# Kernel tuning notes

Measured on AMD Instinct MI355X. Metric: run time of the kernel, lower is better.

## Reference

```python
import jax, jax.numpy as jnp
import numpy as np

EMBED = 768
HEADS = 12
HEAD_DIM = EMBED // HEADS
FFN = 4 * EMBED
EPS = 1e-5


def setup_inputs() -> dict:
    key = jax.random.key(0)
    ks = jax.random.split(key, 12)
    s = 0.02
    inp = {
        'x': jax.random.normal(ks[0], (1, 4096, EMBED), dtype=jnp.float32),
        'Wq': jax.random.normal(ks[1], (EMBED, EMBED), dtype=jnp.float32) * s,
        'bq': jnp.zeros((EMBED,), jnp.float32),
        'Wk': jax.random.normal(ks[2], (EMBED, EMBED), dtype=jnp.float32) * s,
        'bk': jnp.zeros((EMBED,), jnp.float32),
        'Wv': jax.random.normal(ks[3], (EMBED, EMBED), dtype=jnp.float32) * s,
        'bv': jnp.zeros((EMBED,), jnp.float32),
        'Wo': jax.random.normal(ks[4], (EMBED, EMBED), dtype=jnp.float32) * s,
        'bo': jnp.zeros((EMBED,), jnp.float32),
        'ln1_g': jnp.ones((EMBED,), jnp.float32),
        'ln1_b': jnp.zeros((EMBED,), jnp.float32),
        'W1': jax.random.normal(ks[5], (EMBED, FFN), dtype=jnp.float32) * s,
        'b1': jnp.zeros((FFN,), jnp.float32),
        'W2': jax.random.normal(ks[6], (FFN, EMBED), dtype=jnp.float32) * s,
        'b2': jnp.zeros((EMBED,), jnp.float32),
        'ln2_g': jnp.ones((EMBED,), jnp.float32),
        'ln2_b': jnp.zeros((EMBED,), jnp.float32),
    }
    return inp


def _layernorm(x, g, b):
    mu = jnp.mean(x, axis=-1, keepdims=True)
    var = jnp.mean(jnp.square(x - mu), axis=-1, keepdims=True)
    return (x - mu) * jax.lax.rsqrt(var + EPS) * g + b


def reference(x, Wq, bq, Wk, bk, Wv, bv, Wo, bo, ln1_g, ln1_b, W1, b1, W2, b2, ln2_g, ln2_b):
    B, S, D = x.shape
    # QKV projections -> [B, H, S, d]
    def split_heads(t):
        return t.reshape(B, S, HEADS, HEAD_DIM).transpose(0, 2, 1, 3)
    q = split_heads(x @ Wq + bq)
    k = split_heads(x @ Wk + bk)
    v = split_heads(x @ Wv + bv)
    scores = jnp.einsum('bhqd,bhkd->bhqk', q, k) / np.sqrt(HEAD_DIM).astype(np.float32)
    attn = jax.nn.softmax(scores, axis=-1)
    ctx = jnp.einsum('bhqk,bhkd->bhqd', attn, v)
    ctx = ctx.transpose(0, 2, 1, 3).reshape(B, S, D)
    attn_out = ctx @ Wo + bo
    h = _layernorm(x + attn_out, ln1_g, ln1_b)
    ffn = jax.nn.gelu(h @ W1 + b1, approximate=False) @ W2 + b2
    return _layernorm(h + ffn, ln2_g, ln2_b)
```

## Files before the change

kernel.cpp:

```cpp
#include <hip/hip_runtime.h>
#include <hip/hip_bf16.h>

typedef __attribute__((ext_vector_type(8))) short s16x8;
typedef __attribute__((ext_vector_type(4))) int   i32x4;
typedef __attribute__((ext_vector_type(4))) float f32x4;
typedef __attribute__((ext_vector_type(8))) __bf16 bf16x8;

__device__ __forceinline__ short f2bf(float f) {
  unsigned u = __builtin_bit_cast(unsigned, f);
  u = (u + 0x7FFFu + ((u >> 16) & 1u)) >> 16;
  return (short)u;
}
__device__ __forceinline__ float bf2f(short s) {
  unsigned u = ((unsigned)(unsigned short)s) << 16;
  return __builtin_bit_cast(float, u);
}
__device__ __forceinline__ f32x4 mfma16(s16x8 a, s16x8 b, f32x4 c) {
  return __builtin_amdgcn_mfma_f32_16x16x32_bf16(
      __builtin_bit_cast(bf16x8, a), __builtin_bit_cast(bf16x8, b), c, 0, 0, 0);
}
__device__ __forceinline__ void gload16(const void* g, void* l) {
  __builtin_amdgcn_global_load_lds(
      (const __attribute__((address_space(1))) void*)g,
      (__attribute__((address_space(3))) void*)l, 16, 0, 0);
}

__global__ __launch_bounds__(256) void convert_x_kernel(const float* __restrict__ src,
                                                        short* __restrict__ dst, int n8) {
  int i = blockIdx.x * 256 + threadIdx.x;
  if (i >= n8) return;
  float4 v0 = ((const float4*)src)[i * 2];
  float4 v1 = ((const float4*)src)[i * 2 + 1];
  s16x8 o;
  o[0] = f2bf(v0.x); o[1] = f2bf(v0.y); o[2] = f2bf(v0.z); o[3] = f2bf(v0.w);
  o[4] = f2bf(v1.x); o[5] = f2bf(v1.y); o[6] = f2bf(v1.z); o[7] = f2bf(v1.w);
  *(s16x8*)&dst[i * 8] = o;
}

__global__ __launch_bounds__(256) void bconcat_kernel(const float* __restrict__ bq,
                                                      const float* __restrict__ bk,
                                                      const float* __restrict__ bv,
                                                      float* __restrict__ out) {
  int i = blockIdx.x * 256 + threadIdx.x;
  if (i < 2304) out[i] = i < 768 ? bq[i] : (i < 1536 ? bk[i - 768] : bv[i - 1536]);
}

__global__ __launch_bounds__(256) void wconv_kernel(const float* __restrict__ src,
                                                    short* __restrict__ dst, int K, int N) {
  __shared__ float t[32][33];
  int n0 = blockIdx.x * 32, k0 = blockIdx.y * 32;
  int tx = threadIdx.x & 31, ty = threadIdx.x >> 5;
#pragma unroll
  for (int r = 0; r < 4; ++r) t[ty + r * 8][tx] = src[(long)(k0 + ty + r * 8) * N + n0 + tx];
  __syncthreads();
#pragma unroll
  for (int r = 0; r < 4; ++r)
    dst[(long)(n0 + ty + r * 8) * K + k0 + tx] = f2bf(t[tx][ty + r * 8]);
}

__global__ __launch_bounds__(256) void vtrans_kernel(const short* __restrict__ qkv,
                                                     short* __restrict__ vt) {
  __shared__ short t[32][34];
  int c0 = blockIdx.x * 32, s0 = blockIdx.y * 32;
  int tx = threadIdx.x & 31, ty = threadIdx.x >> 5;
#pragma unroll
  for (int r = 0; r < 4; ++r)
    t[ty + r * 8][tx] = qkv[(long)(s0 + ty + r * 8) * 2304 + 1536 + c0 + tx];
  __syncthreads();
#pragma unroll
  for (int r = 0; r < 4; ++r)
    vt[(long)(c0 + ty + r * 8) * 4096 + s0 + tx] = t[tx][ty + r * 8];
}

template <int OUT_MODE>
__global__ __launch_bounds__(256) void gemm_kernel(const short* __restrict__ A,
                                                   const short* __restrict__ Bt,
                                                   const float* __restrict__ bias,
                                                   void* __restrict__ Cout,
                                                   int M, int N, int Kfull, int Ksub) {
  __shared__ short As[128 * 32];
  __shared__ short Bs[128 * 32];
  const int tid = threadIdx.x;
  const int wave = tid >> 6, lane = tid & 63;
  const int lr = lane & 15, lg = lane >> 4;
  const int wm = wave >> 1, wn = wave & 1;
  const int bm = blockIdx.x, bn = blockIdx.y;
  const long koff = (long)blockIdx.z * Ksub;

  f32x4 acc[4][4] = {};

  const int r0 = tid >> 2;
  const int cc = (tid & 3) * 8;
  const short* Ag0 = A + (long)(bm * 128 + r0) * Kfull + koff + cc;
  const short* Ag1 = Ag0 + (long)64 * Kfull;
  const short* Bg0 = Bt + (long)(bn * 128 + r0) * Kfull + koff + cc;
  const short* Bg1 = Bg0 + (long)64 * Kfull;
  short* Asl0 = As + tid * 8;
  short* Asl1 = As + 64 * 32 + tid * 8;
  short* Bsl0 = Bs + tid * 8;
  short* Bsl1 = Bs + 64 * 32 + tid * 8;

  for (int k0 = 0; k0 < Ksub; k0 += 32) {
    __syncthreads();
    gload16(Ag0 + k0, Asl0);
    gload16(Ag1 + k0, Asl1);
    gload16(Bg0 + k0, Bsl0);
    gload16(Bg1 + k0, Bsl1);
    __syncthreads();
    s16x8 af[4], bfr[4];
#pragma unroll
    for (int m = 0; m < 4; ++m) {
      int row = wm * 64 + m * 16 + lr;
      af[m] = *(const s16x8*)&As[row * 32 + lg * 8];
    }
#pragma unroll
    for (int n = 0; n < 4; ++n) {
      int row = wn * 64 + n * 16 + lr;
      bfr[n] = *(const s16x8*)&Bs[row * 32 + lg * 8];
    }
#pragma unroll
    for (int m = 0; m < 4; ++m)
#pragma unroll
      for (int n = 0; n < 4; ++n)
        acc[m][n] = mfma16(af[m], bfr[n], acc[m][n]);
  }

  const int gr0 = bm * 128 + wm * 64 + lg * 4;
  const int gc0 = bn * 128 + wn * 64 + lr;
  float* outF = (float*)Cout + (long)blockIdx.z * M * N;
#pragma unroll
  for (int n = 0; n < 4; ++n) {
    int col = gc0 + n * 16;
    float bb = (blockIdx.z == 0) ? bias[col] : 0.f;
#pragma unroll
    for (int m = 0; m < 4; ++m) {
#pragma unroll
      for (int j = 0; j < 4; ++j) {
        int row = gr0 + m * 16 + j;
        float v = acc[m][n][j] + bb;
        if (OUT_MODE == 2) v = 0.5f * v * (1.0f + erff(v * 0.70710678118f));
        if (OUT_MODE == 1) outF[(long)row * N + col] = v;
        else ((short*)Cout)[(long)row * N + col] = f2bf(v);
      }
    }
  }
}

__global__ __launch_bounds__(256) void flash_kernel(const short* __restrict__ qkv,
                                                    const short* __restrict__ vt,
                                                    float* __restrict__ Opart,
                                                    float* __restrict__ Lpart) {
  __shared__ short Kt[64 * 72];
  __shared__ short Vs[64 * 72];
  __shared__ short Ps[128 * 72];
  const int tid = threadIdx.x;
  const int wave = tid >> 6, lane = tid & 63;
  const int lr = lane & 15, lg = lane >> 4;
  const int h = blockIdx.y, qb = blockIdx.x, sp = blockIdx.z;
  const int qc = h * 64;
  const int hc = 768 + h * 64;
  const int vr = h * 64;
  const float QSCALE = 0.125f * 1.44269504088896f;

#pragma unroll
  for (int i = 0; i < 4; ++i) {
    int c = tid + i * 256;
    int row = c >> 3, cq = (c & 7) * 8;
    *(i32x4*)&Ps[row * 72 + cq] =
        *(const i32x4*)&qkv[(long)(qb * 128 + row) * 2304 + qc + cq];
  }
  __syncthreads();
  s16x8 qf[2][2];
#pragma unroll
  for (int m = 0; m < 2; ++m)
#pragma unroll
    for (int ks = 0; ks < 2; ++ks) {
      int row = wave * 32 + m * 16 + lr;
      s16x8 v = *(const s16x8*)&Ps[row * 72 + ks * 32 + lg * 8];
#pragma unroll
      for (int e = 0; e < 8; ++e) {
        __bf16 b = (__bf16)(bf2f(v[e]) * QSCALE);
        v[e] = (short)__builtin_bit_cast(unsigned short, b);
      }
      qf[m][ks] = v;
    }

  float l_part[8];
#pragma unroll
  for (int i = 0; i < 8; ++i) l_part[i] = 0.f;
  f32x4 oacc[2][4] = {};

  for (int it = 0; it < 32; ++it) {
    const int s0 = sp * 2048 + it * 64;
    __syncthreads();
#pragma unroll
    for (int i = 0; i < 2; ++i) {
      int c = tid + i * 256;
      int row = c >> 3, cq = (c & 7) * 8;
      *(i32x4*)&Kt[row * 72 + cq] =
          *(const i32x4*)&qkv[(long)(s0 + row) * 2304 + hc + cq];
      *(i32x4*)&Vs[row * 72 + cq] =
          *(const i32x4*)&vt[(long)(vr + row) * 4096 + s0 + cq];
    }
    __syncthreads();
    f32x4 sacc[2][4] = {};
#pragma unroll
    for (int ks = 0; ks < 2; ++ks) {
      s16x8 kf[4];
#pragma unroll
      for (int n = 0; n < 4; ++n) {
        int row = n * 16 + lr;
        kf[n] = *(const s16x8*)&Kt[row * 72 + ks * 32 + lg * 8];
      }
      __builtin_amdgcn_s_setprio(1);
#pragma unroll
      for (int m = 0; m < 2; ++m)
#pragma unroll
        for (int n = 0; n < 4; ++n)
          sacc[m][n] = mfma16(qf[m][ks], kf[n], sacc[m][n]);
      __builtin_amdgcn_s_setprio(0);
    }
#pragma unroll
    for (int m = 0; m < 2; ++m) {
#pragma unroll
      for (int j = 0; j < 4; ++j) {
        const int prow = wave * 32 + m * 16 + lg * 4 + j;
        float rs = 0.f;
#pragma unroll
        for (int n = 0; n < 4; ++n) {
          float p = __builtin_amdgcn_exp2f(sacc[m][n][j]);
          rs += p;
          ((__bf16*)Ps)[prow * 72 + n * 16 + lr] = (__bf16)p;
        }
        l_part[m * 4 + j] += rs;
      }
    }
#pragma unroll
    for (int ks = 0; ks < 2; ++ks) {
      s16x8 pf[2], vf[4];
#pragma unroll
      for (int m = 0; m < 2; ++m) {
        int row = wave * 32 + m * 16 + lr;
        pf[m] = *(const s16x8*)&Ps[row * 72 + ks * 32 + lg * 8];
      }
#pragma unroll
      for (int n = 0; n < 4; ++n) {
        int row = n * 16 + lr;
        vf[n] = *(const s16x8*)&Vs[row * 72 + ks * 32 + lg * 8];
      }
      __builtin_amdgcn_s_setprio(1);
#pragma unroll
      for (int m = 0; m < 2; ++m)
#pragma unroll
        for (int n = 0; n < 4; ++n)
          oacc[m][n] = mfma16(pf[m], vf[n], oacc[m][n]);
      __builtin_amdgcn_s_setprio(0);
    }
  }

  const long pbase = ((long)(h * 32 + qb) * 2 + sp) * 128;
#pragma unroll
  for (int m = 0; m < 2; ++m)
#pragma unroll
    for (int j = 0; j < 4; ++j) {
      float l = l_part[m * 4 + j];
      l += __shfl_xor(l, 1);
      l += __shfl_xor(l, 2);
      l += __shfl_xor(l, 4);
      l += __shfl_xor(l, 8);
      if (lr == 0) Lpart[pbase + wave * 32 + m * 16 + lg * 4 + j] = l;
    }
#pragma unroll
  for (int m = 0; m < 2; ++m)
#pragma unroll
    for (int n = 0; n < 4; ++n)
#pragma unroll
      for (int j = 0; j < 4; ++j) {
        int row = wave * 32 + m * 16 + lg * 4 + j;
        Opart[(pbase + row) * 64 + n * 16 + lr] = oacc[m][n][j];
      }
}

__global__ __launch_bounds__(256) void combine_kernel(const float* __restrict__ Opart,
                                                      const float* __restrict__ Lpart,
                                                      short* __restrict__ ctx) {
  const int row = blockIdx.x;
  const int col = blockIdx.y * 256 + threadIdx.x;
  const int h = col >> 6, c = col & 63;
  const int qb = row >> 7, r = row & 127;
  const long p0 = ((long)(h * 32 + qb) * 2) * 128 + r;
  const long p1 = p0 + 128;
  float l = Lpart[p0] + Lpart[p1];
  float o = Opart[p0 * 64 + c] + Opart[p1 * 64 + c];
  ctx[(long)row * 768 + col] = f2bf(o / l);
}

__global__ __launch_bounds__(256) void ln_kernel(const float* __restrict__ a,
                                                 const float* __restrict__ b,
                                                 const float* __restrict__ c,
                                                 const float* __restrict__ g,
                                                 const float* __restrict__ be,
                                                 float* __restrict__ of,
                                                 short* __restrict__ ob) {
  const int row = blockIdx.x;
  const int tid = threadIdx.x;
  const long base = (long)row * 768;
  float v[3];
  float s1 = 0.f, s2 = 0.f;
#pragma unroll
  for (int kk = 0; kk < 3; ++kk) {
    int i = tid + kk * 256;
    float x = a[base + i] + b[base + i] + c[base + i];
    v[kk] = x;
    s1 += x;
    s2 += x * x;
  }
#pragma unroll
  for (int off = 1; off < 64; off <<= 1) {
    s1 += __shfl_xor(s1, off);
    s2 += __shfl_xor(s2, off);
  }
  __shared__ float ws1[4], ws2[4];
  int wave = tid >> 6;
  if ((tid & 63) == 0) { ws1[wave] = s1; ws2[wave] = s2; }
  __syncthreads();
  s1 = ws1[0] + ws1[1] + ws1[2] + ws1[3];
  s2 = ws2[0] + ws2[1] + ws2[2] + ws2[3];
  float mean = s1 * (1.f / 768.f);
  float var = s2 * (1.f / 768.f) - mean * mean;
  float rstd = rsqrtf(var + 1e-5f);
#pragma unroll
  for (int kk = 0; kk < 3; ++kk) {
    int i = tid + kk * 256;
    float o = (v[kk] - mean) * rstd * g[i] + be[i];
    if (of) of[base + i] = o;
    if (ob) ob[base + i] = f2bf(o);
  }
}

extern "C" void kernel_launch(void* const* d_in, const int* in_sizes, int n_in,
                              void* d_out, int out_size, void* d_ws, size_t ws_size,
                              hipStream_t stream) {
  const float* x   = (const float*)d_in[0];
  const float* Wq  = (const float*)d_in[1];
  const float* bq  = (const float*)d_in[2];
  const float* Wk  = (const float*)d_in[3];
  const float* bk  = (const float*)d_in[4];
  const float* Wv  = (const float*)d_in[5];
  const float* bv  = (const float*)d_in[6];
  const float* Wo  = (const float*)d_in[7];
  const float* bo  = (const float*)d_in[8];
  const float* g1  = (const float*)d_in[9];
  const float* be1 = (const float*)d_in[10];
  const float* W1  = (const float*)d_in[11];
  const float* b1  = (const float*)d_in[12];
  const float* W2  = (const float*)d_in[13];
  const float* b2  = (const float*)d_in[14];
  const float* g2  = (const float*)d_in[15];
  const float* be2 = (const float*)d_in[16];

  char* ws = (char*)d_ws;
  size_t off = 0;
  auto alloc = [&](size_t bytes) {
    char* p = ws + off;
    off += (bytes + 255) & ~(size_t)255;
    return p;
  };
  short* xb     = (short*)alloc(4096ul * 768 * 2);
  short* wqkv_t = (short*)alloc(2304ul * 768 * 2);
  short* wo_t   = (short*)alloc(768ul * 768 * 2);
  short* w1_t   = (short*)alloc(3072ul * 768 * 2);
  short* w2_t   = (short*)alloc(768ul * 3072 * 2);
  float* bqkv   = (float*)alloc(2304ul * 4);
  short* qkv    = (short*)alloc(4096ul * 2304 * 2);
  short* vt     = (short*)alloc(768ul * 4096 * 2);
  short* ctx    = (short*)alloc(4096ul * 768 * 2);
  float* attn_o = (float*)alloc(4096ul * 768 * 4);
  short* h_b    = (short*)alloc(4096ul * 768 * 2);
  float* h_f    = (float*)alloc(4096ul * 768 * 4);
  short* f1     = (short*)alloc(4096ul * 3072 * 2);
  float* Opart  = (float*)f1;
  float* Lpart  = (float*)attn_o;
  float* attn_p = (float*)qkv;
  float* ffn_p  = (float*)qkv;

  convert_x_kernel<<<1536, 256, 0, stream>>>(x, xb, 4096 * 768 / 8);
  bconcat_kernel<<<9, 256, 0, stream>>>(bq, bk, bv, bqkv);
  wconv_kernel<<<dim3(24, 24), 256, 0, stream>>>(Wq, wqkv_t, 768, 768);
  wconv_kernel<<<dim3(24, 24), 256, 0, stream>>>(Wk, wqkv_t + 768 * 768, 768, 768);
  wconv_kernel<<<dim3(24, 24), 256, 0, stream>>>(Wv, wqkv_t + 2 * 768 * 768, 768, 768);
  wconv_kernel<<<dim3(24, 24), 256, 0, stream>>>(Wo, wo_t, 768, 768);
  wconv_kernel<<<dim3(96, 24), 256, 0, stream>>>(W1, w1_t, 768, 3072);
  wconv_kernel<<<dim3(24, 96), 256, 0, stream>>>(W2, w2_t, 3072, 768);

  gemm_kernel<0><<<dim3(32, 18), 256, 0, stream>>>(xb, wqkv_t, bqkv, qkv, 4096, 2304, 768, 768);
  vtrans_kernel<<<dim3(24, 128), 256, 0, stream>>>(qkv, vt);
  flash_kernel<<<dim3(32, 12, 2), 256, 0, stream>>>(qkv, vt, Opart, Lpart);
  combine_kernel<<<dim3(4096, 3), 256, 0, stream>>>(Opart, Lpart, ctx);
  gemm_kernel<1><<<dim3(32, 6, 2), 256, 0, stream>>>(ctx, wo_t, bo, attn_p, 4096, 768, 768, 384);
  ln_kernel<<<4096, 256, 0, stream>>>(x, attn_p, attn_p + 4096ul * 768, g1, be1, h_f, h_b);
  gemm_kernel<2><<<dim3(32, 24), 256, 0, stream>>>(h_b, w1_t, b1, f1, 4096, 3072, 768, 768);
  gemm_kernel<1><<<dim3(32, 6, 2), 256, 0, stream>>>(f1, w2_t, b2, ffn_p, 4096, 768, 3072, 1536);
  ln_kernel<<<4096, 256, 0, stream>>>(h_f, ffn_p, ffn_p + 4096ul * 768, g2, be2, (float*)d_out, nullptr);
}
```

Measured before the change: 262.4 us.

## Double-buffer GEMM and flash-attention tiles with async LDS loads and swizzle

The GEMM main loop now keeps two LDS buffers. It prefetches the next K tile with global_load_lds while computing the current one, and uses manual vmcnt waits and raw barriers in place of two __syncthreads per step. The flash kernel gets the same treatment for its K and V^T tiles: they are loaded asynchronously straight into LDS, double-buffered, and laid out unpadded with an XOR chunk swizzle to avoid bank conflicts. The goal is to hide global memory latency behind MFMA work. The cost is doubled LDS use, which can reduce occupancy, and correctness now depends on hand-written waitcnt and barrier ordering.

```diff
diff --git a/kernel.cpp b/kernel.cpp
--- a/kernel.cpp
+++ b/kernel.cpp
@@ -78,8 +78,8 @@
                                                    const float* __restrict__ bias,
                                                    void* __restrict__ Cout,
                                                    int M, int N, int Kfull, int Ksub) {
-  __shared__ short As[128 * 32];
-  __shared__ short Bs[128 * 32];
+  __shared__ short As[2][128 * 32];
+  __shared__ short Bs[2][128 * 32];
   const int tid = threadIdx.x;
   const int wave = tid >> 6, lane = tid & 63;
   const int lr = lane & 15, lg = lane >> 4;
@@ -95,35 +95,48 @@
   const short* Ag1 = Ag0 + (long)64 * Kfull;
   const short* Bg0 = Bt + (long)(bn * 128 + r0) * Kfull + koff + cc;
   const short* Bg1 = Bg0 + (long)64 * Kfull;
-  short* Asl0 = As + tid * 8;
-  short* Asl1 = As + 64 * 32 + tid * 8;
-  short* Bsl0 = Bs + tid * 8;
-  short* Bsl1 = Bs + 64 * 32 + tid * 8;
-
-  for (int k0 = 0; k0 < Ksub; k0 += 32) {
-    __syncthreads();
-    gload16(Ag0 + k0, Asl0);
-    gload16(Ag1 + k0, Asl1);
-    gload16(Bg0 + k0, Bsl0);
-    gload16(Bg1 + k0, Bsl1);
-    __syncthreads();
+
+  auto STAGE = [&](int buf, int k0) {
+    gload16(Ag0 + k0, &As[buf][tid * 8]);
+    gload16(Ag1 + k0, &As[buf][64 * 32 + tid * 8]);
+    gload16(Bg0 + k0, &Bs[buf][tid * 8]);
+    gload16(Bg1 + k0, &Bs[buf][64 * 32 + tid * 8]);
+  };
+  auto COMPUTE = [&](int buf) {
     s16x8 af[4], bfr[4];
 #pragma unroll
     for (int m = 0; m < 4; ++m) {
       int row = wm * 64 + m * 16 + lr;
-      af[m] = *(const s16x8*)&As[row * 32 + lg * 8];
+      af[m] = *(const s16x8*)&As[buf][row * 32 + lg * 8];
     }
 #pragma unroll
     for (int n = 0; n < 4; ++n) {
       int row = wn * 64 + n * 16 + lr;
-      bfr[n] = *(const s16x8*)&Bs[row * 32 + lg * 8];
+      bfr[n] = *(const s16x8*)&Bs[buf][row * 32 + lg * 8];
     }
 #pragma unroll
     for (int m = 0; m < 4; ++m)
 #pragma unroll
       for (int n = 0; n < 4; ++n)
         acc[m][n] = mfma16(af[m], bfr[n], acc[m][n]);
-  }
+  };
+
+  const int nt = Ksub >> 5;
+  STAGE(0, 0);
+  int cur = 0;
+  for (int t = 0; t < nt - 1; ++t) {
+    STAGE(cur ^ 1, (t + 1) * 32);
+    asm volatile("s_waitcnt vmcnt(4)" ::: "memory");
+    __builtin_amdgcn_s_barrier();
+    __builtin_amdgcn_sched_barrier(0);
+    COMPUTE(cur);
+    __builtin_amdgcn_s_barrier();
+    cur ^= 1;
+  }
+  asm volatile("s_waitcnt vmcnt(0)" ::: "memory");
+  __builtin_amdgcn_s_barrier();
+  __builtin_amdgcn_sched_barrier(0);
+  COMPUTE(cur);
 
   const int gr0 = bm * 128 + wm * 64 + lg * 4;
   const int gc0 = bn * 128 + wn * 64 + lr;
@@ -150,8 +163,8 @@
                                                     const short* __restrict__ vt,
                                                     float* __restrict__ Opart,
                                                     float* __restrict__ Lpart) {
-  __shared__ short Kt[64 * 72];
-  __shared__ short Vs[64 * 72];
+  __shared__ short Kt[2][64 * 64];
+  __shared__ short Vs[2][64 * 64];
   __shared__ short Ps[128 * 72];
   const int tid = threadIdx.x;
   const int wave = tid >> 6, lane = tid & 63;
@@ -162,6 +175,17 @@
   const int vr = h * 64;
   const float QSCALE = 0.125f * 1.44269504088896f;
 
+  auto STAGEKV = [&](int buf, int s0) {
+#pragma unroll
+    for (int i = 0; i < 2; ++i) {
+      int c = tid + i * 256;
+      int row = c >> 3;
+      int ch = (c & 7) ^ (row & 7);
+      gload16(&qkv[(long)(s0 + row) * 2304 + hc + ch * 8], &Kt[buf][c * 8]);
+      gload16(&vt[(long)(vr + row) * 4096 + s0 + ch * 8], &Vs[buf][c * 8]);
+    }
+  };
+
 #pragma unroll
   for (int i = 0; i < 4; ++i) {
     int c = tid + i * 256;
@@ -169,6 +193,7 @@
     *(i32x4*)&Ps[row * 72 + cq] =
         *(const i32x4*)&qkv[(long)(qb * 128 + row) * 2304 + qc + cq];
   }
+  STAGEKV(0, sp * 2048);
   __syncthreads();
   s16x8 qf[2][2];
 #pragma unroll
@@ -190,19 +215,17 @@
   for (int i = 0; i < 8; ++i) l_part[i] = 0.f;
   f32x4 oacc[2][4] = {};
 
+  int cur = 0;
   for (int it = 0; it < 32; ++it) {
-    const int s0 = sp * 2048 + it * 64;
-    __syncthreads();
-#pragma unroll
-    for (int i = 0; i < 2; ++i) {
-      int c = tid + i * 256;
-      int row = c >> 3, cq = (c & 7) * 8;
-      *(i32x4*)&Kt[row * 72 + cq] =
-          *(const i32x4*)&qkv[(long)(s0 + row) * 2304 + hc + cq];
-      *(i32x4*)&Vs[row * 72 + cq] =
-          *(const i32x4*)&vt[(long)(vr + row) * 4096 + s0 + cq];
-    }
-    __syncthreads();
+    if (it != 31) {
+      STAGEKV(cur ^ 1, sp * 2048 + (it + 1) * 64);
+      asm volatile("s_waitcnt vmcnt(4)" ::: "memory");
+    } else {
+      asm volatile("s_waitcnt vmcnt(0)" ::: "memory");
+    }
+    __builtin_amdgcn_s_barrier();
+    __builtin_amdgcn_sched_barrier(0);
+
     f32x4 sacc[2][4] = {};
 #pragma unroll
     for (int ks = 0; ks < 2; ++ks) {
@@ -210,7 +233,8 @@
 #pragma unroll
       for (int n = 0; n < 4; ++n) {
         int row = n * 16 + lr;
-        kf[n] = *(const s16x8*)&Kt[row * 72 + ks * 32 + lg * 8];
+        int chk = (ks * 4 + lg) ^ (lr & 7);
+        kf[n] = *(const s16x8*)&Kt[cur][row * 64 + chk * 8];
       }
       __builtin_amdgcn_s_setprio(1);
 #pragma unroll
@@ -246,7 +270,8 @@
 #pragma unroll
       for (int n = 0; n < 4; ++n) {
         int row = n * 16 + lr;
-        vf[n] = *(const s16x8*)&Vs[row * 72 + ks * 32 + lg * 8];
+        int chk = (ks * 4 + lg) ^ (lr & 7);
+        vf[n] = *(const s16x8*)&Vs[cur][row * 64 + chk * 8];
       }
       __builtin_amdgcn_s_setprio(1);
 #pragma unroll
@@ -256,6 +281,8 @@
           oacc[m][n] = mfma16(pf[m], vf[n], oacc[m][n]);
       __builtin_amdgcn_s_setprio(0);
     }
+    __builtin_amdgcn_s_barrier();
+    cur ^= 1;
   }
 
   const long pbase = ((long)(h * 32 + qb) * 2 + sp) * 128;
```

Result: no change. 264.0 us (+0.6%).
